# Kernel tuning notes

Measured on AMD Instinct MI355X. Metric: run time of the kernel, lower is better.

## Reference

```python
import jax, jax.numpy as jnp
from jax import lax
import numpy as np

NUM_EMBEDDINGS = 512
EMBEDDING_DIM = 64
COMMITMENT_COST = 0.25
SPARSITY_LEVEL = 8


def batch_omp(data, dictionary, max_nonzero):
    """Batch-OMP (Rubinstein et al.).
    data: [D, N], dictionary: [D, K] (columns unit-norm). Returns gamma [K, N].
    Runs a fixed max_nonzero greedy steps (the torch tolerance 1e-7 never
    triggers early exit on random data).
    """
    D, N = data.shape
    K = dictionary.shape[1]
    G = dictionary.T @ dictionary                 # [K, K] Gram matrix
    h_bar = (dictionary.T @ data).T               # [N, K] initial correlations
    h = h_bar
    mask = jnp.zeros((N, K), dtype=bool)          # selected-atom indicator
    rows = jnp.arange(N)
    L = jnp.ones((N, 1, 1), dtype=data.dtype)     # incremental Cholesky of G[I,I]
    I = None                                      # [N, k] selected indices
    x = jnp.zeros((N, K), dtype=data.dtype)
    for k in range(1, max_nonzero + 1):
        # greedy atom selection (masking already-chosen atoms)
        idx = jnp.argmax(jnp.abs(h * (~mask).astype(h.dtype)), axis=1)   # [N]
        mask = mask.at[rows, idx].set(True)
        if k > 1:
            g = G[I, idx[:, None]][..., None]                            # [N, k-1, 1]
            w = lax.linalg.triangular_solve(L, g, left_side=True, lower=True)
            w = jnp.swapaxes(w, 1, 2)                                    # [N, 1, k-1]
            w_corner = jnp.sqrt(1.0 - jnp.sum(w * w, axis=2, keepdims=True))
            top = jnp.concatenate([L, jnp.zeros((N, k - 1, 1), L.dtype)], axis=2)
            bot = jnp.concatenate([w, w_corner], axis=2)
            L = jnp.concatenate([top, bot], axis=1)                      # [N, k, k]
            I = jnp.concatenate([I, idx[:, None]], axis=1)
        else:
            I = idx[:, None]
        hb = jnp.take_along_axis(h_bar, I, axis=1)[..., None]            # [N, k, 1]
        # cholesky_solve: L L^T x = hb
        y = lax.linalg.triangular_solve(L, hb, left_side=True, lower=True)
        xs = lax.linalg.triangular_solve(L, y, left_side=True, lower=True,
                                         transpose_a=True)              # [N, k, 1]
        x = jnp.zeros((N, K), data.dtype).at[rows[:, None], I].set(xs[..., 0])
        beta = x @ G                                                     # x is zero off-support
        h = h_bar - beta
    return x.T                                                           # [K, N]


def setup_inputs() -> dict:
    key = jax.random.key(0)
    k1, k2 = jax.random.split(key)
    z_e = jax.random.normal(k1, (32, EMBEDDING_DIM, 32, 32), dtype=jnp.float32)
    dictionary = jax.random.normal(k2, (EMBEDDING_DIM, NUM_EMBEDDINGS), dtype=jnp.float32)
    beta = jnp.array([1.0 - COMMITMENT_COST], dtype=jnp.float32)  # nn.Parameter(1 - commitment_cost)
    return {"z_e": z_e, "dictionary": dictionary, "beta": beta}


def reference(z_e, dictionary, beta):
    # straight-through column normalization (torch does it via .data assignment)
    Dn_val = dictionary / jnp.linalg.norm(dictionary, axis=0)
    Dn = dictionary + lax.stop_gradient(Dn_val - dictionary)
    zp = jnp.transpose(z_e, (0, 2, 3, 1))                 # [B, H, W, C]
    ze_shape = zp.shape
    zf = zp.reshape(EMBEDDING_DIM, -1)                    # view(D, -1): [D, N]
    gamma = lax.stop_gradient(batch_omp(zf, Dn, SPARSITY_LEVEL))   # [K, N]; copied via .data in torch
    recon = Dn @ gamma                                    # [D, N]
    e_latent_loss = jnp.mean((lax.stop_gradient(recon) - zf) ** 2)
    q_loss = jnp.mean((recon - lax.stop_gradient(zf)) ** 2)
    loss = e_latent_loss * COMMITMENT_COST + beta[0] * q_loss
    recon_st = zf + lax.stop_gradient(recon - zf)         # straight-through
    sm = jax.nn.softmax(gamma, axis=0)
    perplexity = jnp.exp(-jnp.mean(jnp.sum(sm * jnp.log(sm + 1e-10), axis=0)))
    recon_out = jnp.transpose(recon_st.reshape(ze_shape), (0, 3, 1, 2))
    return loss, recon_out, lax.stop_gradient(zf), perplexity, gamma
```

## Files before the change

kernel.cpp:

```cpp
#include <hip/hip_runtime.h>
#include <math.h>

#define NCOL 32768
#define KAT  512
#define DIM  64

#define O_LOSS  0
#define O_RECON 1
#define O_ZF    2097153
#define O_PERP  4194305
#define O_GAMMA 4194306

#define WS_DN   0
#define WS_DNT  32768
#define WS_G    65536
#define WS_ACC  327680

__device__ __forceinline__ float wave_max_bcast_f32(float v) {
    int x = __float_as_int(v);
    int t;
    t = __builtin_amdgcn_update_dpp(x, x, 0x111, 0xf, 0xf, false);
    x = __float_as_int(fmaxf(__int_as_float(x), __int_as_float(t)));
    t = __builtin_amdgcn_update_dpp(x, x, 0x112, 0xf, 0xf, false);
    x = __float_as_int(fmaxf(__int_as_float(x), __int_as_float(t)));
    t = __builtin_amdgcn_update_dpp(x, x, 0x114, 0xf, 0xf, false);
    x = __float_as_int(fmaxf(__int_as_float(x), __int_as_float(t)));
    t = __builtin_amdgcn_update_dpp(x, x, 0x118, 0xf, 0xf, false);
    x = __float_as_int(fmaxf(__int_as_float(x), __int_as_float(t)));
    t = __builtin_amdgcn_update_dpp(x, x, 0x142, 0xa, 0xf, false);
    x = __float_as_int(fmaxf(__int_as_float(x), __int_as_float(t)));
    t = __builtin_amdgcn_update_dpp(x, x, 0x143, 0xc, 0xf, false);
    x = __float_as_int(fmaxf(__int_as_float(x), __int_as_float(t)));
    return __int_as_float(__builtin_amdgcn_readlane(x, 63));
}

__device__ __forceinline__ unsigned wave_min_bcast_u32(unsigned v) {
    int x = (int)v;
    int t;
    t = __builtin_amdgcn_update_dpp(x, x, 0x111, 0xf, 0xf, false);
    x = (int)min((unsigned)x, (unsigned)t);
    t = __builtin_amdgcn_update_dpp(x, x, 0x112, 0xf, 0xf, false);
    x = (int)min((unsigned)x, (unsigned)t);
    t = __builtin_amdgcn_update_dpp(x, x, 0x114, 0xf, 0xf, false);
    x = (int)min((unsigned)x, (unsigned)t);
    t = __builtin_amdgcn_update_dpp(x, x, 0x118, 0xf, 0xf, false);
    x = (int)min((unsigned)x, (unsigned)t);
    t = __builtin_amdgcn_update_dpp(x, x, 0x142, 0xa, 0xf, false);
    x = (int)min((unsigned)x, (unsigned)t);
    t = __builtin_amdgcn_update_dpp(x, x, 0x143, 0xc, 0xf, false);
    x = (int)min((unsigned)x, (unsigned)t);
    return (unsigned)__builtin_amdgcn_readlane(x, 63);
}

__global__ void prep_kernel(const float* __restrict__ dict, float* __restrict__ ws) {
    float* Dn  = ws + WS_DN;
    float* DnT = ws + WS_DNT;
    float* acc = ws + WS_ACC;
    int a = threadIdx.x;
    if (a < 2) acc[a] = 0.f;
    float s = 0.f;
    #pragma unroll
    for (int d = 0; d < DIM; ++d) { float v = dict[d*KAT + a]; s += v * v; }
    float nrm = sqrtf(s);
    #pragma unroll
    for (int d = 0; d < DIM; ++d) {
        float v = dict[d*KAT + a] / nrm;
        Dn[d*KAT + a]  = v;
        DnT[a*DIM + d] = v;
    }
}

__global__ void gram_kernel(const float* __restrict__ ws_in, float* __restrict__ ws) {
    const float* Dn = ws_in + WS_DN;
    float* G = ws + WS_G;
    int i = blockIdx.x, j = threadIdx.x;
    float s = 0.f;
    #pragma unroll
    for (int d = 0; d < DIM; ++d)
        s = fmaf(Dn[d*KAT + i], Dn[d*KAT + j], s);
    G[i*KAT + j] = s;
}

__global__ __launch_bounds__(256) void zf_kernel(const float* __restrict__ z_e,
                                                 float* __restrict__ out) {
    __shared__ float tile[64 * 33];
    int s = blockIdx.x;
    int b = s >> 5, h = s & 31;
    int t = threadIdx.x;
    int srcbase = b * 65536 + h * 32;
    #pragma unroll
    for (int i = 0; i < 8; ++i) {
        int e = t + i * 256;
        int c = e >> 5, w = e & 31;
        tile[c * 33 + w] = z_e[srcbase + c * 1024 + w];
    }
    __syncthreads();
    int obase = O_ZF + s * 2048;
    #pragma unroll
    for (int i = 0; i < 8; ++i) {
        int e = t + i * 256;
        out[obase + e] = tile[(e & 63) * 33 + (e >> 6)];
    }
}

__global__ void gzero_kernel(float2* __restrict__ g2) {
    int id = blockIdx.x * 256 + threadIdx.x;
    #pragma unroll
    for (int i = 0; i < 4; ++i)
        g2[id + i * 2097152] = make_float2(0.f, 0.f);
}

__global__ __launch_bounds__(256) void omp_kernel(const float* __restrict__ z_e,
                                                  const float* __restrict__ ws,
                                                  float* __restrict__ out,
                                                  float* __restrict__ wsw) {
    const float* Dn  = ws + WS_DN;
    const float* DnT = ws + WS_DNT;
    const float* G   = ws + WS_G;
    float* acc = wsw + WS_ACC;

    __shared__ float xcols[DIM * 16];
    __shared__ float hbar[16 * KAT];

    const int t = threadIdx.x;
    const int n_base = blockIdx.x * 16;

    #pragma unroll
    for (int i = 0; i < 4; ++i) {
        int e = t + i * 256;
        int d = e >> 4, c = e & 15;
        int L = d * NCOL + n_base + c;
        int src = (L >> 16) * 65536 + (L & 63) * 1024 + (((L >> 11) & 31) << 5) + ((L >> 6) & 31);
        xcols[e] = z_e[src];
    }
    __syncthreads();

    {
        float a0[16], a1[16];
        #pragma unroll
        for (int i = 0; i < 16; ++i) { a0[i] = 0.f; a1[i] = 0.f; }
        const float4* xc4 = (const float4*)xcols;
        for (int d = 0; d < DIM; ++d) {
            float v0 = Dn[d * KAT + t];
            float v1 = Dn[d * KAT + 256 + t];
            #pragma unroll
            for (int q = 0; q < 4; ++q) {
                float4 xv = xc4[d * 4 + q];
                a0[q*4+0] = fmaf(v0, xv.x, a0[q*4+0]);
                a0[q*4+1] = fmaf(v0, xv.y, a0[q*4+1]);
                a0[q*4+2] = fmaf(v0, xv.z, a0[q*4+2]);
                a0[q*4+3] = fmaf(v0, xv.w, a0[q*4+3]);
                a1[q*4+0] = fmaf(v1, xv.x, a1[q*4+0]);
                a1[q*4+1] = fmaf(v1, xv.y, a1[q*4+1]);
                a1[q*4+2] = fmaf(v1, xv.z, a1[q*4+2]);
                a1[q*4+3] = fmaf(v1, xv.w, a1[q*4+3]);
            }
        }
        #pragma unroll
        for (int c = 0; c < 16; ++c) {
            hbar[c * KAT + t]       = a0[c];
            hbar[c * KAT + 256 + t] = a1[c];
        }
    }
    __syncthreads();

    const int wv = t >> 6, lane = t & 63;
    float wv_sq = 0.f, wv_S = 0.f;

    #pragma unroll 1
    for (int cc = 0; cc < 4; ++cc) {
        const int col = wv * 4 + cc;
        const int n = n_base + col;
        const float* hbcol = hbar + col * KAT;

        float h[8];
        #pragma unroll
        for (int r = 0; r < 8; ++r) h[r] = hbcol[(r << 6) + lane];

        unsigned msk = 0;
        float uv[56];
        float Lr[28];
        float invd[8], yv[8], xr[8];
        int Iv[8];

        #pragma unroll
        for (int k = 0; k < 8; ++k) {
            float bv = -1.f; int bi = 0; float hb = 0.f;
            #pragma unroll
            for (int r = 0; r < 8; ++r) {
                float av = ((msk >> r) & 1) ? -1.f : fabsf(h[r]);
                bool gt = av > bv;
                bv = gt ? av : bv;
                bi = gt ? ((r << 6) | lane) : bi;
                hb = gt ? h[r] : hb;
            }
            float maxv = wave_max_bcast_f32(bv);
            unsigned cand = (bv == maxv) ? (unsigned)bi : 0xffffffffu;
            const int idx = (int)wave_min_bcast_u32(cand);
            unsigned long long sm = __ballot((bv == maxv) && (bi == idx) && (hb < 0.f));
            float hwin = (sm != 0ull) ? -maxv : maxv;

            if ((idx & 63) == lane) msk |= 1u << (idx >> 6);
            Iv[k] = idx;

            const float* grow = G + idx * KAT;
            float gk[8];
            if (k < 7) {
                #pragma unroll
                for (int r = 0; r < 8; ++r) gk[r] = grow[(r << 6) + lane];
            }

            float Lk[7];
            if (k == 0) {
                invd[0] = 1.f;
            } else {
                float s2 = 0.f;
                #pragma unroll
                for (int i = 0; i < 7; ++i) if (i < k) {
                    float a = grow[Iv[i]];
                    #pragma unroll
                    for (int j = 0; j < 7; ++j) if (j < i) a = fmaf(-Lr[i*(i-1)/2 + j], Lk[j], a);
                    Lk[i] = a * invd[i];
                    s2 = fmaf(Lk[i], Lk[i], s2);
                }
                #pragma unroll
                for (int j = 0; j < 7; ++j) if (j < k) Lr[k*(k-1)/2 + j] = Lk[j];
                invd[k] = 1.f / sqrtf(1.f - s2);
            }
            yv[k] = hwin * invd[k];

            if (k < 7) {
                #pragma unroll
                for (int r = 0; r < 8; ++r) {
                    float a = gk[r];
                    #pragma unroll
                    for (int j = 0; j < 7; ++j) if (j < k) a = fmaf(-Lk[j], uv[j*8 + r], a);
                    a *= invd[k];
                    uv[k*8 + r] = a;
                    h[r] = fmaf(-yv[k], a, h[r]);
                }
            }
        }

        #pragma unroll
        for (int i = 7; i >= 0; --i) {
            float a = yv[i];
            #pragma unroll
            for (int j = 0; j < 8; ++j) if (j > i) a = fmaf(-Lr[j*(j-1)/2 + i], xr[j], a);
            xr[i] = a * invd[i];
        }

        #pragma unroll
        for (int j = 0; j < 8; ++j)
            if (lane == j) out[O_GAMMA + Iv[j] * NCOL + n] = xr[j];

        float rec = 0.f;
        #pragma unroll
        for (int j = 0; j < 8; ++j)
            rec = fmaf(xr[j], DnT[Iv[j] * DIM + lane], rec);
        int L = lane * NCOL + n;
        int perm = (L >> 16) * 65536 + (L & 63) * 1024 + (((L >> 11) & 31) << 5) + ((L >> 6) & 31);
        out[O_RECON + perm] = rec;

        float xd = xcols[lane * 16 + col];
        float diff = rec - xd;
        float sq = diff * diff;
        #pragma unroll
        for (int off = 32; off; off >>= 1) sq += __shfl_xor(sq, off, 64);
        if (lane == 0) wv_sq += sq;

        {
            float m = 0.f;
            #pragma unroll
            for (int j = 0; j < 8; ++j) m = fmaxf(m, xr[j]);
            float xsel = 0.f;
            #pragma unroll
            for (int j = 0; j < 8; ++j) xsel = (lane == j) ? xr[j] : xsel;
            float e = (lane < 8) ? expf(xsel - m) : 0.f;
            float se = e;
            #pragma unroll
            for (int off = 1; off < 8; off <<= 1) se += __shfl_xor(se, off, 64);
            float e0 = expf(-m);
            float Z = fmaf(504.f, e0, se);
            float invZ = 1.f / Z;
            float p = e * invZ;
            float tq = (lane < 8) ? p * logf(p + 1e-10f) : 0.f;
            #pragma unroll
            for (int off = 1; off < 8; off <<= 1) tq += __shfl_xor(tq, off, 64);
            if (lane == 0) {
                float p0 = e0 * invZ;
                wv_S += tq + 504.f * p0 * logf(p0 + 1e-10f);
            }
        }
    }

    if (lane == 0) {
        atomicAdd(&acc[0], wv_sq);
        atomicAdd(&acc[1], wv_S);
    }
}

__global__ void fin_kernel(const float* __restrict__ ws, const float* __restrict__ beta,
                           float* __restrict__ out) {
    const float* acc = ws + WS_ACC;
    float mse = acc[0] / 2097152.f;
    out[O_LOSS] = mse * 0.25f + beta[0] * mse;
    out[O_PERP] = expf(-acc[1] / 32768.f);
}

extern "C" void kernel_launch(void* const* d_in, const int* in_sizes, int n_in,
                              void* d_out, int out_size, void* d_ws, size_t ws_size,
                              hipStream_t stream) {
    const float* z_e  = (const float*)d_in[0];
    const float* dict = (const float*)d_in[1];
    const float* beta = (const float*)d_in[2];
    float* out = (float*)d_out;
    float* ws  = (float*)d_ws;

    prep_kernel<<<1, 512, 0, stream>>>(dict, ws);
    gram_kernel<<<512, 512, 0, stream>>>(ws, ws);
    zf_kernel<<<1024, 256, 0, stream>>>(z_e, out);
    gzero_kernel<<<8192, 256, 0, stream>>>((float2*)(out + O_GAMMA));
    omp_kernel<<<2048, 256, 0, stream>>>(z_e, ws, out, ws);
    fin_kernel<<<1, 1, 0, stream>>>(ws, beta, out);
}
```

Before: 370.0 us.

## Halve OMP columns per block, merge zf/gzero kernels, add DPP reductions and argmax fast path

Cuts OMP columns per block from 16 to 8, which doubles the grid to 4096 blocks and reduces shared memory per block so more blocks can be resident. The zf transpose and gamma zeroing kernels are merged into one launch, and prep_kernel is spread across 8 blocks. Shuffle-based wave reductions are replaced with DPP sum reductions. The argmax gains a single-winner fast path using readlane, skipping the min reduction when there is no tie. In exchange, each block recomputes the h_bar GEMV over fewer columns, so Dn reuse per global load drops and the dictionary is read from global memory more often.

```diff
diff --git a/kernel.cpp b/kernel.cpp
--- a/kernel.cpp
+++ b/kernel.cpp
@@ -4,6 +4,7 @@
 #define NCOL 32768
 #define KAT  512
 #define DIM  64
+#define CPB  8
 
 #define O_LOSS  0
 #define O_RECON 1
@@ -52,12 +53,42 @@
     return (unsigned)__builtin_amdgcn_readlane(x, 63);
 }
 
+__device__ __forceinline__ float wave_sum_bcast_f32(float v) {
+    int x = __float_as_int(v);
+    int t;
+    t = __builtin_amdgcn_update_dpp(x, x, 0x0B1, 0xf, 0xf, false);
+    x = __float_as_int(__int_as_float(x) + __int_as_float(t));
+    t = __builtin_amdgcn_update_dpp(x, x, 0x04E, 0xf, 0xf, false);
+    x = __float_as_int(__int_as_float(x) + __int_as_float(t));
+    t = __builtin_amdgcn_update_dpp(x, x, 0x141, 0xf, 0xf, false);
+    x = __float_as_int(__int_as_float(x) + __int_as_float(t));
+    t = __builtin_amdgcn_update_dpp(x, x, 0x140, 0xf, 0xf, false);
+    x = __float_as_int(__int_as_float(x) + __int_as_float(t));
+    t = __builtin_amdgcn_update_dpp(x, x, 0x142, 0xa, 0xf, false);
+    x = __float_as_int(__int_as_float(x) + __int_as_float(t));
+    t = __builtin_amdgcn_update_dpp(x, x, 0x143, 0xc, 0xf, false);
+    x = __float_as_int(__int_as_float(x) + __int_as_float(t));
+    return __int_as_float(__builtin_amdgcn_readlane(x, 63));
+}
+
+__device__ __forceinline__ float sum8_all_f32(float v) {
+    int x = __float_as_int(v);
+    int t;
+    t = __builtin_amdgcn_update_dpp(x, x, 0x0B1, 0xf, 0xf, false);
+    x = __float_as_int(__int_as_float(x) + __int_as_float(t));
+    t = __builtin_amdgcn_update_dpp(x, x, 0x04E, 0xf, 0xf, false);
+    x = __float_as_int(__int_as_float(x) + __int_as_float(t));
+    t = __builtin_amdgcn_update_dpp(x, x, 0x141, 0xf, 0xf, false);
+    x = __float_as_int(__int_as_float(x) + __int_as_float(t));
+    return __int_as_float(x);
+}
+
 __global__ void prep_kernel(const float* __restrict__ dict, float* __restrict__ ws) {
     float* Dn  = ws + WS_DN;
     float* DnT = ws + WS_DNT;
     float* acc = ws + WS_ACC;
-    int a = threadIdx.x;
-    if (a < 2) acc[a] = 0.f;
+    int a = blockIdx.x * 64 + threadIdx.x;
+    if (blockIdx.x == 0 && threadIdx.x < 2) acc[threadIdx.x] = 0.f;
     float s = 0.f;
     #pragma unroll
     for (int d = 0; d < DIM; ++d) { float v = dict[d*KAT + a]; s += v * v; }
@@ -81,33 +112,34 @@
     G[i*KAT + j] = s;
 }
 
-__global__ __launch_bounds__(256) void zf_kernel(const float* __restrict__ z_e,
+__global__ __launch_bounds__(256) void zg_kernel(const float* __restrict__ z_e,
                                                  float* __restrict__ out) {
     __shared__ float tile[64 * 33];
-    int s = blockIdx.x;
-    int b = s >> 5, h = s & 31;
     int t = threadIdx.x;
-    int srcbase = b * 65536 + h * 32;
-    #pragma unroll
-    for (int i = 0; i < 8; ++i) {
-        int e = t + i * 256;
-        int c = e >> 5, w = e & 31;
-        tile[c * 33 + w] = z_e[srcbase + c * 1024 + w];
-    }
-    __syncthreads();
-    int obase = O_ZF + s * 2048;
-    #pragma unroll
-    for (int i = 0; i < 8; ++i) {
-        int e = t + i * 256;
-        out[obase + e] = tile[(e & 63) * 33 + (e >> 6)];
-    }
-}
-
-__global__ void gzero_kernel(float2* __restrict__ g2) {
-    int id = blockIdx.x * 256 + threadIdx.x;
-    #pragma unroll
-    for (int i = 0; i < 4; ++i)
-        g2[id + i * 2097152] = make_float2(0.f, 0.f);
+    if (blockIdx.x < 1024) {
+        int s = blockIdx.x;
+        int b = s >> 5, h = s & 31;
+        int srcbase = b * 65536 + h * 32;
+        #pragma unroll
+        for (int i = 0; i < 8; ++i) {
+            int e = t + i * 256;
+            int c = e >> 5, w = e & 31;
+            tile[c * 33 + w] = z_e[srcbase + c * 1024 + w];
+        }
+        __syncthreads();
+        int obase = O_ZF + s * 2048;
+        #pragma unroll
+        for (int i = 0; i < 8; ++i) {
+            int e = t + i * 256;
+            out[obase + e] = tile[(e & 63) * 33 + (e >> 6)];
+        }
+    } else {
+        float2* g2 = (float2*)(out + O_GAMMA);
+        int id = (blockIdx.x - 1024) * 256 + t;
+        #pragma unroll
+        for (int i = 0; i < 4; ++i)
+            g2[id + i * 2097152] = make_float2(0.f, 0.f);
+    }
 }
 
 __global__ __launch_bounds__(256) void omp_kernel(const float* __restrict__ z_e,
@@ -119,16 +151,16 @@
     const float* G   = ws + WS_G;
     float* acc = wsw + WS_ACC;
 
-    __shared__ float xcols[DIM * 16];
-    __shared__ float hbar[16 * KAT];
+    __shared__ __align__(16) float xcols[DIM * CPB];
+    __shared__ float hbar[CPB * KAT];
 
     const int t = threadIdx.x;
-    const int n_base = blockIdx.x * 16;
+    const int n_base = blockIdx.x * CPB;
 
     #pragma unroll
-    for (int i = 0; i < 4; ++i) {
+    for (int i = 0; i < 2; ++i) {
         int e = t + i * 256;
-        int d = e >> 4, c = e & 15;
+        int d = e >> 3, c = e & 7;
         int L = d * NCOL + n_base + c;
         int src = (L >> 16) * 65536 + (L & 63) * 1024 + (((L >> 11) & 31) << 5) + ((L >> 6) & 31);
         xcols[e] = z_e[src];
@@ -136,28 +168,34 @@
     __syncthreads();
 
     {
-        float a0[16], a1[16];
-        #pragma unroll
-        for (int i = 0; i < 16; ++i) { a0[i] = 0.f; a1[i] = 0.f; }
+        float a0[8], a1[8];
+        #pragma unroll
+        for (int i = 0; i < 8; ++i) { a0[i] = 0.f; a1[i] = 0.f; }
         const float4* xc4 = (const float4*)xcols;
         for (int d = 0; d < DIM; ++d) {
             float v0 = Dn[d * KAT + t];
             float v1 = Dn[d * KAT + 256 + t];
-            #pragma unroll
-            for (int q = 0; q < 4; ++q) {
-                float4 xv = xc4[d * 4 + q];
-                a0[q*4+0] = fmaf(v0, xv.x, a0[q*4+0]);
-                a0[q*4+1] = fmaf(v0, xv.y, a0[q*4+1]);
-                a0[q*4+2] = fmaf(v0, xv.z, a0[q*4+2]);
-                a0[q*4+3] = fmaf(v0, xv.w, a0[q*4+3]);
-                a1[q*4+0] = fmaf(v1, xv.x, a1[q*4+0]);
-                a1[q*4+1] = fmaf(v1, xv.y, a1[q*4+1]);
-                a1[q*4+2] = fmaf(v1, xv.z, a1[q*4+2]);
-                a1[q*4+3] = fmaf(v1, xv.w, a1[q*4+3]);
-            }
-        }
-        #pragma unroll
-        for (int c = 0; c < 16; ++c) {
+            float4 xa = xc4[d * 2 + 0];
+            float4 xb = xc4[d * 2 + 1];
+            a0[0] = fmaf(v0, xa.x, a0[0]);
+            a0[1] = fmaf(v0, xa.y, a0[1]);
+            a0[2] = fmaf(v0, xa.z, a0[2]);
+            a0[3] = fmaf(v0, xa.w, a0[3]);
+            a0[4] = fmaf(v0, xb.x, a0[4]);
+            a0[5] = fmaf(v0, xb.y, a0[5]);
+            a0[6] = fmaf(v0, xb.z, a0[6]);
+            a0[7] = fmaf(v0, xb.w, a0[7]);
+            a1[0] = fmaf(v1, xa.x, a1[0]);
+            a1[1] = fmaf(v1, xa.y, a1[1]);
+            a1[2] = fmaf(v1, xa.z, a1[2]);
+            a1[3] = fmaf(v1, xa.w, a1[3]);
+            a1[4] = fmaf(v1, xb.x, a1[4]);
+            a1[5] = fmaf(v1, xb.y, a1[5]);
+            a1[6] = fmaf(v1, xb.z, a1[6]);
+            a1[7] = fmaf(v1, xb.w, a1[7]);
+        }
+        #pragma unroll
+        for (int c = 0; c < 8; ++c) {
             hbar[c * KAT + t]       = a0[c];
             hbar[c * KAT + 256 + t] = a1[c];
         }
@@ -168,8 +206,8 @@
     float wv_sq = 0.f, wv_S = 0.f;
 
     #pragma unroll 1
-    for (int cc = 0; cc < 4; ++cc) {
-        const int col = wv * 4 + cc;
+    for (int cc = 0; cc < 2; ++cc) {
+        const int col = wv * 2 + cc;
         const int n = n_base + col;
         const float* hbcol = hbar + col * KAT;
 
@@ -195,10 +233,18 @@
                 hb = gt ? h[r] : hb;
             }
             float maxv = wave_max_bcast_f32(bv);
-            unsigned cand = (bv == maxv) ? (unsigned)bi : 0xffffffffu;
-            const int idx = (int)wave_min_bcast_u32(cand);
-            unsigned long long sm = __ballot((bv == maxv) && (bi == idx) && (hb < 0.f));
-            float hwin = (sm != 0ull) ? -maxv : maxv;
+            unsigned long long tie = __ballot(bv == maxv);
+            int idx; float hwin;
+            if (__popcll(tie) == 1) {
+                int sl = __ffsll((unsigned long long)tie) - 1;
+                idx  = __builtin_amdgcn_readlane(bi, sl);
+                hwin = __int_as_float(__builtin_amdgcn_readlane(__float_as_int(hb), sl));
+            } else {
+                unsigned cand = (bv == maxv) ? (unsigned)bi : 0xffffffffu;
+                idx = (int)wave_min_bcast_u32(cand);
+                unsigned long long sm = __ballot((bv == maxv) && (bi == idx) && (hb < 0.f));
+                hwin = (sm != 0ull) ? -maxv : maxv;
+            }
 
             if ((idx & 63) == lane) msk |= 1u << (idx >> 6);
             Iv[k] = idx;
@@ -262,12 +308,9 @@
         int perm = (L >> 16) * 65536 + (L & 63) * 1024 + (((L >> 11) & 31) << 5) + ((L >> 6) & 31);
         out[O_RECON + perm] = rec;
 
-        float xd = xcols[lane * 16 + col];
+        float xd = xcols[lane * CPB + col];
         float diff = rec - xd;
-        float sq = diff * diff;
-        #pragma unroll
-        for (int off = 32; off; off >>= 1) sq += __shfl_xor(sq, off, 64);
-        if (lane == 0) wv_sq += sq;
+        wv_sq += wave_sum_bcast_f32(diff * diff);
 
         {
             float m = 0.f;
@@ -277,16 +320,13 @@
             #pragma unroll
             for (int j = 0; j < 8; ++j) xsel = (lane == j) ? xr[j] : xsel;
             float e = (lane < 8) ? expf(xsel - m) : 0.f;
-            float se = e;
-            #pragma unroll
-            for (int off = 1; off < 8; off <<= 1) se += __shfl_xor(se, off, 64);
+            float se = sum8_all_f32(e);
             float e0 = expf(-m);
             float Z = fmaf(504.f, e0, se);
             float invZ = 1.f / Z;
             float p = e * invZ;
             float tq = (lane < 8) ? p * logf(p + 1e-10f) : 0.f;
-            #pragma unroll
-            for (int off = 1; off < 8; off <<= 1) tq += __shfl_xor(tq, off, 64);
+            tq = sum8_all_f32(tq);
             if (lane == 0) {
                 float p0 = e0 * invZ;
                 wv_S += tq + 504.f * p0 * logf(p0 + 1e-10f);
@@ -317,10 +357,9 @@
     float* out = (float*)d_out;
     float* ws  = (float*)d_ws;
 
-    prep_kernel<<<1, 512, 0, stream>>>(dict, ws);
+    prep_kernel<<<8, 64, 0, stream>>>(dict, ws);
     gram_kernel<<<512, 512, 0, stream>>>(ws, ws);
-    zf_kernel<<<1024, 256, 0, stream>>>(z_e, out);
-    gzero_kernel<<<8192, 256, 0, stream>>>((float2*)(out + O_GAMMA));
-    omp_kernel<<<2048, 256, 0, stream>>>(z_e, ws, out, ws);
+    zg_kernel<<<9216, 256, 0, stream>>>(z_e, out);
+    omp_kernel<<<4096, 256, 0, stream>>>(z_e, ws, out, ws);
     fin_kernel<<<1, 1, 0, stream>>>(ws, beta, out);
 }
```

Measured after the change: 549.9 us. 1.49x slower.
